# Optimization experiments

Measured on AMD Instinct MI355X. Metric: run time of the kernel, lower is better.

## Reference

```python
import jax, jax.numpy as jnp
import numpy as np

N_NODES = 50000
N_EDGES = 800000
F_IN = 128
HID = 256


def setup_inputs() -> dict:
    key = jax.random.key(0)
    ks = jax.random.split(key, 10)
    x = jax.random.normal(ks[0], (N_NODES, F_IN), jnp.float32)
    edge_index = jax.random.randint(ks[1], (2, N_EDGES), 0, N_NODES, jnp.int32)
    # Glorot-ish scaled weights (PyG Linear default init style)
    def w(k, o, i):
        return jax.random.normal(k, (o, i), jnp.float32) * (1.0 / np.sqrt(i))
    return {
        "x": x,
        "edge_index": edge_index,
        "W1l": w(ks[2], HID, F_IN), "b1l": jnp.zeros((HID,), jnp.float32),
        "W1r": w(ks[3], HID, F_IN),
        "W2l": w(ks[4], HID, HID), "b2l": jnp.zeros((HID,), jnp.float32),
        "W2r": w(ks[5], HID, HID),
        "Wh1": w(ks[6], 4, HID), "bh1": jnp.zeros((4,), jnp.float32),
        "Wh2": w(ks[7], 3, HID), "bh2": jnp.zeros((3,), jnp.float32),
    }


def sage_conv(x, edge_index, Wl, bl, Wr):
    # PyG SAGEConv (aggr='mean'): out_i = Wl @ mean_{j in N(i)} x_j + bl + Wr @ x_i
    src, dst = edge_index[0], edge_index[1]
    n = x.shape[0]
    summed = jax.ops.segment_sum(x[src], dst, num_segments=n)        # [N, F]
    cnt = jax.ops.segment_sum(jnp.ones((src.shape[0],), x.dtype), dst, num_segments=n)
    agg = summed / jnp.maximum(cnt, 1.0)[:, None]                    # isolated nodes -> 0
    return agg @ Wl.T + bl + x @ Wr.T


def reference(x, edge_index, W1l, b1l, W1r, W2l, b2l, W2r, Wh1, bh1, Wh2, bh2):
    h = jax.nn.relu(sage_conv(x, edge_index, W1l, b1l, W1r))
    # dropout(p=0.5) is identity in eval mode
    h = sage_conv(h, edge_index, W2l, b2l, W2r)
    out1 = h @ Wh1.T + bh1   # l2_classifier=False branch
    out2 = h @ Wh2.T + bh2
    return (out1, out2, h)
```

## Files before the change

kernel.cpp:

```cpp
#include <hip/hip_runtime.h>
#include <hip/hip_bf16.h>

typedef short bf16x8 __attribute__((ext_vector_type(8)));
typedef float f32x4 __attribute__((ext_vector_type(4)));

__device__ __forceinline__ float bf2f(__hip_bfloat16 v) { return __bfloat162float(v); }

__global__ void detect_kernel(const unsigned short* __restrict__ xu, int* __restrict__ flag) {
    if (blockIdx.x != 0 || threadIdx.x != 0) return;
    int good = 0;
    for (int i = 0; i < 128; i += 2) {
        unsigned short u = xu[i];
        unsigned e = (u >> 7) & 0xFF;
        if (u == 0 || (e >= 110 && e <= 137)) good++;
    }
    *flag = (good < 32) ? 1 : 0;
}

__device__ __forceinline__ float loadAny(const void* p, size_t i, int isf32) {
    return isf32 ? ((const float*)p)[i] : bf2f(((const __hip_bfloat16*)p)[i]);
}

__global__ void ingest_kernel(const void* __restrict__ src, __hip_bfloat16* __restrict__ dst,
                              int n, const int* __restrict__ flag) {
    int isf32 = *flag;
    int t = blockIdx.x * blockDim.x + threadIdx.x;
    if (t >= n) return;
    dst[t] = __float2bfloat16(loadAny(src, t, isf32));
}

__global__ void prep_kernel(const void* W1l, const void* W1r, const void* W2l, const void* W2r,
                            const void* b1l, const void* b2l, const void* Wh1, const void* Wh2,
                            const void* bh1, const void* bh2,
                            __hip_bfloat16* __restrict__ W1c, __hip_bfloat16* __restrict__ W2c,
                            __hip_bfloat16* __restrict__ sb, const int* __restrict__ flag) {
    int isf32 = *flag;
    int t = blockIdx.x * blockDim.x + threadIdx.x;
    if (t < 65536) {
        int n = t >> 8, k = t & 255;
        float v = (k < 128) ? loadAny(W1l, n * 128 + k, isf32)
                            : loadAny(W1r, n * 128 + (k - 128), isf32);
        W1c[t] = __float2bfloat16(v);
        return;
    }
    int u = t - 65536;
    if (u < 131072) {
        int n = u >> 9, k = u & 511;
        float v = (k < 256) ? loadAny(W2l, n * 256 + k, isf32)
                            : loadAny(W2r, n * 256 + (k - 256), isf32);
        W2c[u] = __float2bfloat16(v);
        return;
    }
    int s = u - 131072;
    float v;
    if      (s < 256)  v = loadAny(b1l, s, isf32);
    else if (s < 512)  v = loadAny(b2l, s - 256, isf32);
    else if (s < 1536) v = loadAny(Wh1, s - 512, isf32);
    else if (s < 2304) v = loadAny(Wh2, s - 1536, isf32);
    else if (s < 2308) v = loadAny(bh1, s - 2304, isf32);
    else if (s < 2311) v = loadAny(bh2, s - 2308, isf32);
    else return;
    sb[s] = __float2bfloat16(v);
}

__global__ void deg_kernel(const int* __restrict__ ei, int E, int* __restrict__ deg) {
    int t = blockIdx.x * blockDim.x + threadIdx.x;
    if (t >= E) return;
    atomicAdd(&deg[ei[E + t]], 1);
}

__global__ __launch_bounds__(256) void scanA_kernel(const int* __restrict__ deg,
                                                    int* __restrict__ off,
                                                    int* __restrict__ bsum, int N) {
    __shared__ int ts[256];
    int t = threadIdx.x;
    int base = blockIdx.x * 1024 + t * 4;
    int v0 = (base + 0 < N) ? deg[base + 0] : 0;
    int v1 = (base + 1 < N) ? deg[base + 1] : 0;
    int v2 = (base + 2 < N) ? deg[base + 2] : 0;
    int v3 = (base + 3 < N) ? deg[base + 3] : 0;
    int i0 = v0, i1 = i0 + v1, i2 = i1 + v2, i3 = i2 + v3;
    ts[t] = i3;
    __syncthreads();
    for (int d = 1; d < 256; d <<= 1) {
        int x = (t >= d) ? ts[t - d] : 0;
        __syncthreads();
        ts[t] += x;
        __syncthreads();
    }
    int excl = (t > 0) ? ts[t - 1] : 0;
    if (base + 0 < N) off[base + 1] = excl + i0;
    if (base + 1 < N) off[base + 2] = excl + i1;
    if (base + 2 < N) off[base + 3] = excl + i2;
    if (base + 3 < N) off[base + 4] = excl + i3;
    if (t == 255) bsum[blockIdx.x] = ts[255];
}

__global__ __launch_bounds__(1024) void scanB_kernel(int* __restrict__ bsum, int nb) {
    __shared__ int ts[1024];
    int t = threadIdx.x;
    ts[t] = (t < nb) ? bsum[t] : 0;
    __syncthreads();
    for (int d = 1; d < 1024; d <<= 1) {
        int x = (t >= d) ? ts[t - d] : 0;
        __syncthreads();
        ts[t] += x;
        __syncthreads();
    }
    if (t < nb) bsum[t] = (t > 0) ? ts[t - 1] : 0;
}

__global__ void addC_kernel(int* __restrict__ off, const int* __restrict__ bsum, int N) {
    int i = blockIdx.x * blockDim.x + threadIdx.x;
    if (i == 0) off[0] = 0;
    if (i < N) off[i + 1] += bsum[i >> 10];
}

__global__ void fill_kernel(const int* __restrict__ ei, int E,
                            const int* __restrict__ off, int* __restrict__ cursor,
                            int* __restrict__ srcs) {
    int t = blockIdx.x * blockDim.x + threadIdx.x;
    if (t >= E) return;
    int dst = ei[E + t];
    int pos = off[dst] + atomicAdd(&cursor[dst], 1);
    srcs[pos] = ei[t];
}

__global__ void gather1_kernel(const __hip_bfloat16* __restrict__ x,
                               const int* __restrict__ off, const int* __restrict__ srcs,
                               __hip_bfloat16* __restrict__ agg, int N) {
    int wid  = (blockIdx.x * blockDim.x + threadIdx.x) >> 6;
    int lane = threadIdx.x & 63;
    if (wid >= N) return;
    int beg = off[wid], end = off[wid + 1];
    float a0 = 0.f, a1 = 0.f;
    const __hip_bfloat162* xb = (const __hip_bfloat162*)x;
    int e = beg;
    for (; e + 3 < end; e += 4) {
        int s0 = srcs[e], s1 = srcs[e + 1], s2 = srcs[e + 2], s3 = srcs[e + 3];
        __hip_bfloat162 u0 = xb[(size_t)s0 * 64 + lane];
        __hip_bfloat162 u1 = xb[(size_t)s1 * 64 + lane];
        __hip_bfloat162 u2 = xb[(size_t)s2 * 64 + lane];
        __hip_bfloat162 u3 = xb[(size_t)s3 * 64 + lane];
        a0 += bf2f(u0.x) + bf2f(u1.x) + bf2f(u2.x) + bf2f(u3.x);
        a1 += bf2f(u0.y) + bf2f(u1.y) + bf2f(u2.y) + bf2f(u3.y);
    }
    for (; e < end; e++) {
        int s = srcs[e];
        __hip_bfloat162 u = xb[(size_t)s * 64 + lane];
        a0 += bf2f(u.x); a1 += bf2f(u.y);
    }
    float inv = 1.0f / fmaxf((float)(end - beg), 1.0f);
    __hip_bfloat162 o;
    o.x = __float2bfloat16(a0 * inv);
    o.y = __float2bfloat16(a1 * inv);
    ((__hip_bfloat162*)agg)[(size_t)wid * 64 + lane] = o;
}

__global__ void gather2_kernel(const __hip_bfloat16* __restrict__ h,
                               const int* __restrict__ off, const int* __restrict__ srcs,
                               __hip_bfloat16* __restrict__ agg, int N) {
    int gid  = blockIdx.x * blockDim.x + threadIdx.x;
    int node = gid >> 7;
    int t    = gid & 127;
    if (node >= N) return;
    int beg = off[node], end = off[node + 1];
    float a0 = 0.f, a1 = 0.f;
    const __hip_bfloat162* hb = (const __hip_bfloat162*)h;
    int e = beg;
    for (; e + 3 < end; e += 4) {
        int s0 = srcs[e], s1 = srcs[e + 1], s2 = srcs[e + 2], s3 = srcs[e + 3];
        __hip_bfloat162 u0 = hb[(size_t)s0 * 128 + t];
        __hip_bfloat162 u1 = hb[(size_t)s1 * 128 + t];
        __hip_bfloat162 u2 = hb[(size_t)s2 * 128 + t];
        __hip_bfloat162 u3 = hb[(size_t)s3 * 128 + t];
        a0 += bf2f(u0.x) + bf2f(u1.x) + bf2f(u2.x) + bf2f(u3.x);
        a1 += bf2f(u0.y) + bf2f(u1.y) + bf2f(u2.y) + bf2f(u3.y);
    }
    for (; e < end; e++) {
        int s = srcs[e];
        __hip_bfloat162 u = hb[(size_t)s * 128 + t];
        a0 += bf2f(u.x); a1 += bf2f(u.y);
    }
    float inv = 1.0f / fmaxf((float)(end - beg), 1.0f);
    __hip_bfloat162 o;
    o.x = __float2bfloat16(a0 * inv);
    o.y = __float2bfloat16(a1 * inv);
    ((__hip_bfloat162*)agg)[(size_t)node * 128 + t] = o;
}

struct AFrag { bf16x8 v[4]; };

template <int K, int KA, bool RELU, bool TOOUT>
__global__ __launch_bounds__(256) void gemm_lds(const __hip_bfloat16* __restrict__ A1,
                                                const __hip_bfloat16* __restrict__ A2, int M,
                                                const __hip_bfloat16* __restrict__ W,
                                                const __hip_bfloat16* __restrict__ bias,
                                                __hip_bfloat16* __restrict__ outb,
                                                void* __restrict__ dout,
                                                const int* __restrict__ flag) {
    __shared__ short wlds[32768];
    constexpr int KB = K - KA;
    constexpr int NCHUNK = K / 256;
    int tid  = threadIdx.x;
    int wave = tid >> 6, lane = tid & 63, quad = lane >> 4, l15 = lane & 15;
    int rowBlk = blockIdx.x >> 1, half = blockIdx.x & 1;
    int R0 = rowBlk * 256;
    int cbase = half * 128;

    int mrow[4];
#pragma unroll
    for (int rt = 0; rt < 4; rt++) mrow[rt] = min(R0 + wave * 64 + rt * 16 + l15, M - 1);

    const short* Ws = (const short*)W;

    auto loadW = [&](int p, bf16x8* wreg) {
#pragma unroll
        for (int i = 0; i < 16; i++) {
            int unit = tid + i * 256;
            int ln = unit & 63, nt = (unit >> 6) & 7, kt = unit >> 9;
            int row = cbase + nt * 16 + (ln & 15);
            int kk  = p * 256 + kt * 32 + (ln >> 4) * 8;
            wreg[i] = *(const bf16x8*)(Ws + (size_t)row * K + kk);
        }
    };
    auto storeW = [&](const bf16x8* wreg) {
#pragma unroll
        for (int i = 0; i < 16; i++) {
            int unit = tid + i * 256;
            *(bf16x8*)&wlds[unit * 8] = wreg[i];
        }
    };
    auto loadA = [&](int kglob) {
        AFrag f;
#pragma unroll
        for (int rt = 0; rt < 4; rt++) {
            const short* ap = (kglob < KA)
                ? (const short*)A1 + (size_t)mrow[rt] * KA + kglob + quad * 8
                : (const short*)A2 + (size_t)mrow[rt] * KB + (kglob - KA) + quad * 8;
            f.v[rt] = *(const bf16x8*)ap;
        }
        return f;
    };

    f32x4 acc[4][8];
#pragma unroll
    for (int rt = 0; rt < 4; rt++)
#pragma unroll
        for (int nt = 0; nt < 8; nt++) acc[rt][nt] = {0.f, 0.f, 0.f, 0.f};

    bf16x8 wreg[16];
    loadW(0, wreg);
    storeW(wreg);
    __syncthreads();
    AFrag a_cur = loadA(0);

    for (int p = 0; p < NCHUNK; p++) {
        if (p + 1 < NCHUNK) loadW(p + 1, wreg);
#pragma unroll
        for (int kt = 0; kt < 8; kt++) {
            int kg = p * 256 + kt * 32;
            int kg_next = (kg + 32 < K) ? (kg + 32) : kg;
            AFrag a_next = loadA(kg_next);
#pragma unroll
            for (int nt = 0; nt < 8; nt++) {
                bf16x8 b = *(const bf16x8*)&wlds[((kt * 8 + nt) * 64 + lane) * 8];
#pragma unroll
                for (int rt = 0; rt < 4; rt++)
                    acc[rt][nt] = __builtin_amdgcn_mfma_f32_16x16x32_bf16(a_cur.v[rt], b, acc[rt][nt], 0, 0, 0);
            }
            a_cur = a_next;
        }
        if (p + 1 < NCHUNK) {
            __syncthreads();
            storeW(wreg);
            __syncthreads();
        }
    }

    int isf32 = TOOUT ? *flag : 0;
    float* hf = TOOUT ? ((float*)dout + (size_t)M * 7) : nullptr;
    __hip_bfloat16* hb = TOOUT ? ((__hip_bfloat16*)dout + (size_t)M * 7) : outb;

#pragma unroll
    for (int rt = 0; rt < 4; rt++) {
#pragma unroll
        for (int nt = 0; nt < 8; nt++) {
            int col = cbase + nt * 16 + l15;
            float bv = bf2f(bias[col]);
#pragma unroll
            for (int r = 0; r < 4; r++) {
                int row = R0 + wave * 64 + rt * 16 + quad * 4 + r;
                if (row < M) {
                    float v = acc[rt][nt][r] + bv;
                    if (RELU) v = fmaxf(v, 0.f);
                    size_t idx = (size_t)row * 256 + col;
                    if (TOOUT && isf32) hf[idx] = v;
                    else                hb[idx] = __float2bfloat16(v);
                }
            }
        }
    }
}

__global__ void heads_kernel(const __hip_bfloat16* __restrict__ sb,
                             void* dout, int N, const int* __restrict__ flag) {
    int isf32 = *flag;
    int node = (blockIdx.x * blockDim.x + threadIdx.x) >> 6;
    int lane = threadIdx.x & 63;
    if (node >= N) return;
    float hv0, hv1, hv2, hv3;
    if (isf32) {
        const float4* hp = (const float4*)((const float*)dout + (size_t)N * 7);
        float4 v = hp[(size_t)node * 64 + lane];
        hv0 = v.x; hv1 = v.y; hv2 = v.z; hv3 = v.w;
    } else {
        const __hip_bfloat162* hp = (const __hip_bfloat162*)((const __hip_bfloat16*)dout + (size_t)N * 7);
        __hip_bfloat162 a = hp[(size_t)node * 128 + 2 * lane];
        __hip_bfloat162 b = hp[(size_t)node * 128 + 2 * lane + 1];
        hv0 = bf2f(a.x); hv1 = bf2f(a.y); hv2 = bf2f(b.x); hv3 = bf2f(b.y);
    }
#pragma unroll
    for (int r = 0; r < 7; r++) {
        const __hip_bfloat16* wrow = (r < 4) ? (sb + 512 + r * 256) : (sb + 1536 + (r - 4) * 256);
        const __hip_bfloat162* wr2 = (const __hip_bfloat162*)wrow;
        __hip_bfloat162 wa = wr2[2 * lane];
        __hip_bfloat162 wb = wr2[2 * lane + 1];
        float p = hv0 * bf2f(wa.x) + hv1 * bf2f(wa.y) + hv2 * bf2f(wb.x) + hv3 * bf2f(wb.y);
        for (int off = 32; off > 0; off >>= 1) p += __shfl_down(p, off, 64);
        if (lane == 0) {
            float bias = (r < 4) ? bf2f(sb[2304 + r]) : bf2f(sb[2308 + (r - 4)]);
            float v = p + bias;
            size_t idx = (r < 4) ? ((size_t)node * 4 + r)
                                 : ((size_t)N * 4 + (size_t)node * 3 + (r - 4));
            if (isf32) ((float*)dout)[idx] = v;
            else       ((__hip_bfloat16*)dout)[idx] = __float2bfloat16(v);
        }
    }
}

extern "C" void kernel_launch(void* const* d_in, const int* in_sizes, int n_in,
                              void* d_out, int out_size, void* d_ws, size_t ws_size,
                              hipStream_t stream) {
    const void* x   = d_in[0];
    const int*  ei  = (const int*)d_in[1];
    const void* W1l = d_in[2];
    const void* b1l = d_in[3];
    const void* W1r = d_in[4];
    const void* W2l = d_in[5];
    const void* b2l = d_in[6];
    const void* W2r = d_in[7];
    const void* Wh1 = d_in[8];
    const void* bh1 = d_in[9];
    const void* Wh2 = d_in[10];
    const void* bh2 = d_in[11];

    const int N = in_sizes[0] / 128;
    const int E = in_sizes[1] / 2;
    const int NB = (N + 1023) / 1024;

    char* ws = (char*)d_ws;
    int*            offp   = (int*)(ws + 0);
    int*            deg    = (int*)(ws + 262144);
    int*            cursor = (int*)(ws + 524288);
    int*            bsum   = (int*)(ws + 724992);
    int*            srcs   = (int*)(ws + 786432);
    __hip_bfloat16* W1c    = (__hip_bfloat16*)(ws + 3986432);
    __hip_bfloat16* W2c    = (__hip_bfloat16*)(ws + 4117504);
    __hip_bfloat16* sb     = (__hip_bfloat16*)(ws + 4379648);
    __hip_bfloat16* xn     = (__hip_bfloat16*)(ws + 4387840);
    __hip_bfloat16* h1     = (__hip_bfloat16*)(ws + 17187840);
    __hip_bfloat16* agg    = (__hip_bfloat16*)(ws + 42787840);
    int*            flag   = (int*)(ws + 68387840);

    hipMemsetAsync(ws + 262144, 0, 524288, stream);

    detect_kernel<<<1, 64, 0, stream>>>((const unsigned short*)x, flag);

    ingest_kernel<<<(N * 128 + 255) / 256, 256, 0, stream>>>(x, xn, N * 128, flag);
    prep_kernel<<<(65536 + 131072 + 2311 + 255) / 256, 256, 0, stream>>>(
        W1l, W1r, W2l, W2r, b1l, b2l, Wh1, Wh2, bh1, bh2, W1c, W2c, sb, flag);

    deg_kernel<<<(E + 255) / 256, 256, 0, stream>>>(ei, E, deg);
    scanA_kernel<<<NB, 256, 0, stream>>>(deg, offp, bsum, N);
    scanB_kernel<<<1, 1024, 0, stream>>>(bsum, NB);
    addC_kernel<<<(N + 255) / 256, 256, 0, stream>>>(offp, bsum, N);
    fill_kernel<<<(E + 255) / 256, 256, 0, stream>>>(ei, E, offp, cursor, srcs);

    const int rowBlks = (N + 255) / 256;

    gather1_kernel<<<(N + 3) / 4, 256, 0, stream>>>(xn, offp, srcs, agg, N);
    gemm_lds<256, 128, true, false><<<rowBlks * 2, 256, 0, stream>>>(
        agg, xn, N, W1c, sb, h1, nullptr, flag);

    gather2_kernel<<<(N * 128 + 255) / 256, 256, 0, stream>>>(h1, offp, srcs, agg, N);
    gemm_lds<512, 256, false, true><<<rowBlks * 2, 256, 0, stream>>>(
        agg, h1, N, W2c, sb + 256, nullptr, d_out, flag);

    heads_kernel<<<(N + 3) / 4, 256, 0, stream>>>(sb, d_out, N, flag);
}
```

Measured before the change: 407.6 us.

## Vectorize gathers and ingest to 8-byte loads, deepen A-prefetch, wave-ballot detect

```diff
diff --git a/kernel.cpp b/kernel.cpp
--- a/kernel.cpp
+++ b/kernel.cpp
@@ -5,16 +5,20 @@
 typedef float f32x4 __attribute__((ext_vector_type(4)));
 
 __device__ __forceinline__ float bf2f(__hip_bfloat16 v) { return __bfloat162float(v); }
+__device__ __forceinline__ float sh2f(short s) {
+    union { float f; unsigned u; } c; c.u = ((unsigned)(unsigned short)s) << 16; return c.f;
+}
+__device__ __forceinline__ short f2sh(float f) {
+    __hip_bfloat16 b = __float2bfloat16(f); return *(short*)&b;
+}
 
 __global__ void detect_kernel(const unsigned short* __restrict__ xu, int* __restrict__ flag) {
-    if (blockIdx.x != 0 || threadIdx.x != 0) return;
-    int good = 0;
-    for (int i = 0; i < 128; i += 2) {
-        unsigned short u = xu[i];
-        unsigned e = (u >> 7) & 0xFF;
-        if (u == 0 || (e >= 110 && e <= 137)) good++;
-    }
-    *flag = (good < 32) ? 1 : 0;
+    int lane = threadIdx.x;
+    unsigned short u = xu[lane * 2];
+    unsigned e = (u >> 7) & 0xFF;
+    bool good = (u == 0) || (e >= 110 && e <= 137);
+    unsigned long long m = __ballot(good);
+    if (lane == 0) *flag = (__popcll(m) < 32) ? 1 : 0;
 }
 
 __device__ __forceinline__ float loadAny(const void* p, size_t i, int isf32) {
@@ -22,11 +26,18 @@
 }
 
 __global__ void ingest_kernel(const void* __restrict__ src, __hip_bfloat16* __restrict__ dst,
-                              int n, const int* __restrict__ flag) {
+                              int n4, const int* __restrict__ flag) {
     int isf32 = *flag;
     int t = blockIdx.x * blockDim.x + threadIdx.x;
-    if (t >= n) return;
-    dst[t] = __float2bfloat16(loadAny(src, t, isf32));
+    if (t >= n4) return;
+    short4 o;
+    if (isf32) {
+        float4 v = ((const float4*)src)[t];
+        o.x = f2sh(v.x); o.y = f2sh(v.y); o.z = f2sh(v.z); o.w = f2sh(v.w);
+    } else {
+        o = ((const short4*)src)[t];
+    }
+    ((short4*)dst)[t] = o;
 }
 
 __global__ void prep_kernel(const void* W1l, const void* W1r, const void* W2l, const void* W2r,
@@ -129,64 +140,66 @@
 __global__ void gather1_kernel(const __hip_bfloat16* __restrict__ x,
                                const int* __restrict__ off, const int* __restrict__ srcs,
                                __hip_bfloat16* __restrict__ agg, int N) {
-    int wid  = (blockIdx.x * blockDim.x + threadIdx.x) >> 6;
+    int gid  = blockIdx.x * blockDim.x + threadIdx.x;
+    int wid  = gid >> 6;
     int lane = threadIdx.x & 63;
-    if (wid >= N) return;
-    int beg = off[wid], end = off[wid + 1];
-    float a0 = 0.f, a1 = 0.f;
-    const __hip_bfloat162* xb = (const __hip_bfloat162*)x;
+    int node = wid * 2 + (lane >> 5);
+    int t    = lane & 31;
+    if (node >= N) return;
+    int beg = off[node], end = off[node + 1];
+    float a0 = 0.f, a1 = 0.f, a2 = 0.f, a3 = 0.f;
+    const short4* xb = (const short4*)x;
     int e = beg;
-    for (; e + 3 < end; e += 4) {
-        int s0 = srcs[e], s1 = srcs[e + 1], s2 = srcs[e + 2], s3 = srcs[e + 3];
-        __hip_bfloat162 u0 = xb[(size_t)s0 * 64 + lane];
-        __hip_bfloat162 u1 = xb[(size_t)s1 * 64 + lane];
-        __hip_bfloat162 u2 = xb[(size_t)s2 * 64 + lane];
-        __hip_bfloat162 u3 = xb[(size_t)s3 * 64 + lane];
-        a0 += bf2f(u0.x) + bf2f(u1.x) + bf2f(u2.x) + bf2f(u3.x);
-        a1 += bf2f(u0.y) + bf2f(u1.y) + bf2f(u2.y) + bf2f(u3.y);
+    for (; e + 7 < end; e += 8) {
+        short4 v[8];
+#pragma unroll
+        for (int j = 0; j < 8; j++) v[j] = xb[(size_t)srcs[e + j] * 32 + t];
+#pragma unroll
+        for (int j = 0; j < 8; j++) {
+            a0 += sh2f(v[j].x); a1 += sh2f(v[j].y);
+            a2 += sh2f(v[j].z); a3 += sh2f(v[j].w);
+        }
     }
     for (; e < end; e++) {
-        int s = srcs[e];
-        __hip_bfloat162 u = xb[(size_t)s * 64 + lane];
-        a0 += bf2f(u.x); a1 += bf2f(u.y);
+        short4 v = xb[(size_t)srcs[e] * 32 + t];
+        a0 += sh2f(v.x); a1 += sh2f(v.y); a2 += sh2f(v.z); a3 += sh2f(v.w);
     }
     float inv = 1.0f / fmaxf((float)(end - beg), 1.0f);
-    __hip_bfloat162 o;
-    o.x = __float2bfloat16(a0 * inv);
-    o.y = __float2bfloat16(a1 * inv);
-    ((__hip_bfloat162*)agg)[(size_t)wid * 64 + lane] = o;
+    short4 o;
+    o.x = f2sh(a0 * inv); o.y = f2sh(a1 * inv);
+    o.z = f2sh(a2 * inv); o.w = f2sh(a3 * inv);
+    ((short4*)agg)[(size_t)node * 32 + t] = o;
 }
 
 __global__ void gather2_kernel(const __hip_bfloat16* __restrict__ h,
                                const int* __restrict__ off, const int* __restrict__ srcs,
                                __hip_bfloat16* __restrict__ agg, int N) {
-    int gid  = blockIdx.x * blockDim.x + threadIdx.x;
-    int node = gid >> 7;
-    int t    = gid & 127;
+    int node = (blockIdx.x * blockDim.x + threadIdx.x) >> 6;
+    int lane = threadIdx.x & 63;
     if (node >= N) return;
     int beg = off[node], end = off[node + 1];
-    float a0 = 0.f, a1 = 0.f;
-    const __hip_bfloat162* hb = (const __hip_bfloat162*)h;
+    float a0 = 0.f, a1 = 0.f, a2 = 0.f, a3 = 0.f;
+    const short4* hb = (const short4*)h;
     int e = beg;
-    for (; e + 3 < end; e += 4) {
-        int s0 = srcs[e], s1 = srcs[e + 1], s2 = srcs[e + 2], s3 = srcs[e + 3];
-        __hip_bfloat162 u0 = hb[(size_t)s0 * 128 + t];
-        __hip_bfloat162 u1 = hb[(size_t)s1 * 128 + t];
-        __hip_bfloat162 u2 = hb[(size_t)s2 * 128 + t];
-        __hip_bfloat162 u3 = hb[(size_t)s3 * 128 + t];
-        a0 += bf2f(u0.x) + bf2f(u1.x) + bf2f(u2.x) + bf2f(u3.x);
-        a1 += bf2f(u0.y) + bf2f(u1.y) + bf2f(u2.y) + bf2f(u3.y);
+    for (; e + 7 < end; e += 8) {
+        short4 v[8];
+#pragma unroll
+        for (int j = 0; j < 8; j++) v[j] = hb[(size_t)srcs[e + j] * 64 + lane];
+#pragma unroll
+        for (int j = 0; j < 8; j++) {
+            a0 += sh2f(v[j].x); a1 += sh2f(v[j].y);
+            a2 += sh2f(v[j].z); a3 += sh2f(v[j].w);
+        }
     }
     for (; e < end; e++) {
-        int s = srcs[e];
-        __hip_bfloat162 u = hb[(size_t)s * 128 + t];
-        a0 += bf2f(u.x); a1 += bf2f(u.y);
+        short4 v = hb[(size_t)srcs[e] * 64 + lane];
+        a0 += sh2f(v.x); a1 += sh2f(v.y); a2 += sh2f(v.z); a3 += sh2f(v.w);
     }
     float inv = 1.0f / fmaxf((float)(end - beg), 1.0f);
-    __hip_bfloat162 o;
-    o.x = __float2bfloat16(a0 * inv);
-    o.y = __float2bfloat16(a1 * inv);
-    ((__hip_bfloat162*)agg)[(size_t)node * 128 + t] = o;
+    short4 o;
+    o.x = f2sh(a0 * inv); o.y = f2sh(a1 * inv);
+    o.z = f2sh(a2 * inv); o.w = f2sh(a3 * inv);
+    ((short4*)agg)[(size_t)node * 64 + lane] = o;
 }
 
 struct AFrag { bf16x8 v[4]; };
@@ -253,23 +266,26 @@
     loadW(0, wreg);
     storeW(wreg);
     __syncthreads();
-    AFrag a_cur = loadA(0);
+    AFrag a0f = loadA(0);
+    AFrag a1f = loadA(32 < K ? 32 : 0);
 
     for (int p = 0; p < NCHUNK; p++) {
         if (p + 1 < NCHUNK) loadW(p + 1, wreg);
 #pragma unroll
         for (int kt = 0; kt < 8; kt++) {
             int kg = p * 256 + kt * 32;
-            int kg_next = (kg + 32 < K) ? (kg + 32) : kg;
-            AFrag a_next = loadA(kg_next);
+            int kg2 = kg + 64;
+            if (kg2 > K - 32) kg2 = K - 32;
+            AFrag a_next = loadA(kg2);
 #pragma unroll
             for (int nt = 0; nt < 8; nt++) {
                 bf16x8 b = *(const bf16x8*)&wlds[((kt * 8 + nt) * 64 + lane) * 8];
 #pragma unroll
                 for (int rt = 0; rt < 4; rt++)
-                    acc[rt][nt] = __builtin_amdgcn_mfma_f32_16x16x32_bf16(a_cur.v[rt], b, acc[rt][nt], 0, 0, 0);
+                    acc[rt][nt] = __builtin_amdgcn_mfma_f32_16x16x32_bf16(a0f.v[rt], b, acc[rt][nt], 0, 0, 0);
             }
-            a_cur = a_next;
+            a0f = a1f;
+            a1f = a_next;
         }
         if (p + 1 < NCHUNK) {
             __syncthreads();
@@ -377,7 +393,7 @@
 
     detect_kernel<<<1, 64, 0, stream>>>((const unsigned short*)x, flag);
 
-    ingest_kernel<<<(N * 128 + 255) / 256, 256, 0, stream>>>(x, xn, N * 128, flag);
+    ingest_kernel<<<(N * 32 + 255) / 256, 256, 0, stream>>>(x, xn, N * 32, flag);
     prep_kernel<<<(65536 + 131072 + 2311 + 255) / 256, 256, 0, stream>>>(
         W1l, W1r, W2l, W2r, b1l, b2l, Wh1, Wh2, bh1, bh2, W1c, W2c, sb, flag);
 
@@ -389,11 +405,14 @@
 
     const int rowBlks = (N + 255) / 256;
 
-    gather1_kernel<<<(N + 3) / 4, 256, 0, stream>>>(xn, offp, srcs, agg, N);
+    {
+        int waves = (N + 1) / 2;
+        gather1_kernel<<<(waves * 64 + 255) / 256, 256, 0, stream>>>(xn, offp, srcs, agg, N);
+    }
     gemm_lds<256, 128, true, false><<<rowBlks * 2, 256, 0, stream>>>(
         agg, xn, N, W1c, sb, h1, nullptr, flag);
 
-    gather2_kernel<<<(N * 128 + 255) / 256, 256, 0, stream>>>(h1, offp, srcs, agg, N);
+    gather2_kernel<<<(N * 64 + 255) / 256, 256, 0, stream>>>(h1, offp, srcs, agg, N);
     gemm_lds<512, 256, false, true><<<rowBlks * 2, 256, 0, stream>>>(
         agg, h1, N, W2c, sb + 256, nullptr, d_out, flag);
 
```

Measured after the change: 390.9 us. 4.1% less time.
